# Kernel optimization log

Measured on AMD Instinct MI355X. Metric: run time of the kernel, lower is better.

Reference implementation:

```python
import jax, jax.numpy as jnp
import numpy as np

D_MODEL = 1024
D_FF = 4096
LN_EPS = 1e-5


def _layer_norm(x, gamma, beta):
    mu = jnp.mean(x, axis=-1, keepdims=True)
    var = jnp.mean(jnp.square(x - mu), axis=-1, keepdims=True)
    return (x - mu) * jax.lax.rsqrt(var + LN_EPS) * gamma + beta


def setup_inputs() -> dict:
    key = jax.random.key(0)
    ks = jax.random.split(key, 16)
    B, S, D, F = 2, 2048, D_MODEL, D_FF
    s_d = 1.0 / np.sqrt(D)
    s_f = 1.0 / np.sqrt(F)
    u = lambda k, shape, s: jax.random.uniform(k, shape, jnp.float32, -s, s)
    return {
        "x": jax.random.normal(ks[0], (B, S, D), jnp.float32),
        "wq": u(ks[1], (D, D), s_d), "bq": u(ks[2], (D,), s_d),
        "wk": u(ks[3], (D, D), s_d), "bk": u(ks[4], (D,), s_d),
        "wv": u(ks[5], (D, D), s_d), "bv": u(ks[6], (D,), s_d),
        "wo": u(ks[7], (D, D), s_d), "bo": u(ks[8], (D,), s_d),
        "w1": u(ks[9], (F, D), s_d), "b1": u(ks[10], (F,), s_d),
        "w2": u(ks[11], (D, F), s_f), "b2": u(ks[12], (D,), s_f),
        "g1": jnp.ones((D,), jnp.float32), "be1": jnp.zeros((D,), jnp.float32),
        "g2": jnp.ones((D,), jnp.float32), "be2": jnp.zeros((D,), jnp.float32),
        "num_heads": 16,
    }


def reference(x, wq, bq, wk, bk, wv, bv, wo, bo, w1, b1, w2, b2, g1, be1, g2, be2, num_heads):
    B, S, D = x.shape
    H = num_heads
    dk = D // H
    scale = 1.0 / np.sqrt(dk)

    # --- self-attention (pre-norm) ---
    h = _layer_norm(x, g1, be1)
    q = (h @ wq.T + bq).reshape(B, S, H, dk)
    k = (h @ wk.T + bk).reshape(B, S, H, dk)
    v = (h @ wv.T + bv).reshape(B, S, H, dk)
    scores = jnp.einsum("bqhd,bkhd->bhqk", q, k) * scale  # [B,H,S,S]
    attn = jax.nn.softmax(scores, axis=-1)
    ctx = jnp.einsum("bhqk,bkhd->bqhd", attn, v).reshape(B, S, D)
    x = x + ctx @ wo.T + bo

    # --- feed-forward (pre-norm, exact GELU as in torch default) ---
    h = _layer_norm(x, g2, be2)
    h = jax.nn.gelu(h @ w1.T + b1, approximate=False)
    x = x + h @ w2.T + b2
    return x
```

## Files before the change

kernel.cpp:

```cpp
#include <hip/hip_runtime.h>

typedef __attribute__((ext_vector_type(8))) __bf16 bf16x8;
typedef __attribute__((ext_vector_type(4))) __bf16 bf16x4;
typedef __attribute__((ext_vector_type(4))) float floatx4;
typedef void __attribute__((address_space(3))) lds_void_t;
typedef const void __attribute__((address_space(1))) gbl_void_t;

#define D_MODEL 1024
#define SEQ     2048
#define BATCH   2
#define NH      16
#define DK      64
#define DFF     4096
#define NTOK    (BATCH * SEQ)
#define QKVS    3072

__device__ __forceinline__ float gelu_exact(float x) {
    return 0.5f * x * (1.0f + erff(x * 0.70710678118654752f));
}

__global__ __launch_bounds__(256) void cast_f32_bf16(const float* __restrict__ src,
                                                     __bf16* __restrict__ dst, int n) {
    int i = (blockIdx.x * 256 + threadIdx.x) * 8;
    if (i >= n) return;
    floatx4 a = *(const floatx4*)(src + i);
    floatx4 b = *(const floatx4*)(src + i + 4);
    bf16x8 o;
    for (int j = 0; j < 4; ++j) { o[j] = (__bf16)a[j]; o[4 + j] = (__bf16)b[j]; }
    *(bf16x8*)(dst + i) = o;
}

__global__ __launch_bounds__(64) void ln_kernel(const float* __restrict__ x,
                                                const float* __restrict__ g,
                                                const float* __restrict__ b,
                                                __bf16* __restrict__ out) {
    int row = blockIdx.x, lane = threadIdx.x, base = lane * 16;
    const float* xr = x + (size_t)row * D_MODEL + base;
    float v[16];
    for (int j = 0; j < 4; ++j) {
        floatx4 a = *(const floatx4*)(xr + 4 * j);
        for (int i = 0; i < 4; ++i) v[4 * j + i] = a[i];
    }
    float s = 0.f, sq = 0.f;
    for (int i = 0; i < 16; ++i) { s += v[i]; sq += v[i] * v[i]; }
    for (int o = 1; o < 64; o <<= 1) { s += __shfl_xor(s, o); sq += __shfl_xor(sq, o); }
    float mu = s * (1.0f / D_MODEL);
    float var = sq * (1.0f / D_MODEL) - mu * mu;
    float rstd = rsqrtf(fmaxf(var, 0.f) + 1e-5f);

    const floatx4* gp = (const floatx4*)(g + base);
    const floatx4* bp = (const floatx4*)(b + base);
    bf16x8 o0, o1;
    for (int j = 0; j < 2; ++j) {
        floatx4 gv0 = gp[2 * j], gv1 = gp[2 * j + 1];
        floatx4 bv0 = bp[2 * j], bv1 = bp[2 * j + 1];
        for (int i = 0; i < 4; ++i) {
            float r0 = (v[8 * j + i] - mu) * rstd * gv0[i] + bv0[i];
            float r1 = (v[8 * j + 4 + i] - mu) * rstd * gv1[i] + bv1[i];
            if (j == 0) { o0[i] = (__bf16)r0; o0[4 + i] = (__bf16)r1; }
            else        { o1[i] = (__bf16)r0; o1[4 + i] = (__bf16)r1; }
        }
    }
    bf16x8* op = (bf16x8*)(out + (size_t)row * D_MODEL + base);
    op[0] = o0; op[1] = o1;
}

template <typename OutT, bool GELU, bool TRIBIAS, int KSPLIT>
__global__ __launch_bounds__(256) void gemm_bt(const __bf16* __restrict__ A,
                                               const __bf16* __restrict__ W,
                                               const float* __restrict__ bias0,
                                               const float* __restrict__ bias1,
                                               const float* __restrict__ bias2,
                                               const float* __restrict__ res,
                                               OutT* out, float* part1,
                                               int M, int N, int K) {
    __shared__ __bf16 As[2][128][32];
    __shared__ __bf16 Ws[2][128][32];

    int m0 = blockIdx.y * 128, n0 = blockIdx.x * 128;
    int t = threadIdx.x;
    int lane = t & 63, wave = t >> 6;
    int wm = (wave >> 1) * 64, wn = (wave & 1) * 64;
    int fr = lane & 15, quad = lane >> 4;
    int srow = t >> 2, scol = (t & 3) * 8;

    int Ks = K / KSPLIT;
    int kbeg = (KSPLIT > 1) ? blockIdx.z * Ks : 0;

    floatx4 acc[4][4] = {};

    const __bf16* Ab = A + (size_t)(m0 + srow) * K + kbeg + scol;
    const __bf16* Wb = W + (size_t)(n0 + srow) * K + kbeg + scol;

    auto stage = [&](int buf, int k0) {
        __builtin_amdgcn_global_load_lds((gbl_void_t*)(Ab + k0),
                                         (lds_void_t*)&As[buf][wave * 16][0], 16, 0, 0);
        __builtin_amdgcn_global_load_lds((gbl_void_t*)(Ab + (size_t)64 * K + k0),
                                         (lds_void_t*)&As[buf][64 + wave * 16][0], 16, 0, 0);
        __builtin_amdgcn_global_load_lds((gbl_void_t*)(Wb + k0),
                                         (lds_void_t*)&Ws[buf][wave * 16][0], 16, 0, 0);
        __builtin_amdgcn_global_load_lds((gbl_void_t*)(Wb + (size_t)64 * K + k0),
                                         (lds_void_t*)&Ws[buf][64 + wave * 16][0], 16, 0, 0);
    };

    stage(0, 0);
    int nsteps = Ks / 32;
    for (int s = 0; s < nsteps; ++s) {
        int cur = s & 1;
        __syncthreads();
        if (s + 1 < nsteps) stage(cur ^ 1, (s + 1) * 32);

        bf16x8 af[4], wf[4];
#pragma unroll
        for (int i = 0; i < 4; ++i) af[i] = *(const bf16x8*)&As[cur][wm + i * 16 + fr][quad * 8];
#pragma unroll
        for (int i = 0; i < 4; ++i) wf[i] = *(const bf16x8*)&Ws[cur][wn + i * 16 + fr][quad * 8];
#pragma unroll
        for (int mi = 0; mi < 4; ++mi)
#pragma unroll
            for (int ni = 0; ni < 4; ++ni)
                acc[mi][ni] = __builtin_amdgcn_mfma_f32_16x16x32_bf16(af[mi], wf[ni], acc[mi][ni], 0, 0, 0);
    }

    if (KSPLIT > 1) {
        float* pb = (blockIdx.z == 0) ? (float*)out : part1;
#pragma unroll
        for (int ni = 0; ni < 4; ++ni) {
            int col = n0 + wn + ni * 16 + fr;
#pragma unroll
            for (int mi = 0; mi < 4; ++mi)
#pragma unroll
                for (int r = 0; r < 4; ++r) {
                    int row = m0 + wm + mi * 16 + quad * 4 + r;
                    pb[(size_t)row * N + col] = acc[mi][ni][r];
                }
        }
    } else {
#pragma unroll
        for (int ni = 0; ni < 4; ++ni) {
            int col = n0 + wn + ni * 16 + fr;
            const float* bp = bias0;
            int bcol = col;
            if (TRIBIAS) { bp = col < 1024 ? bias0 : (col < 2048 ? bias1 : bias2); bcol = col & 1023; }
            float bv = bp[bcol];
#pragma unroll
            for (int mi = 0; mi < 4; ++mi) {
#pragma unroll
                for (int r = 0; r < 4; ++r) {
                    int row = m0 + wm + mi * 16 + quad * 4 + r;
                    float v = acc[mi][ni][r] + bv;
                    if (GELU) v = gelu_exact(v);
                    if (res) v += res[(size_t)row * N + col];
                    out[(size_t)row * N + col] = (OutT)v;
                }
            }
        }
    }
}

__global__ __launch_bounds__(256) void reduce_k2(const float* __restrict__ p0,
                                                 const float* p1,
                                                 const float* __restrict__ res,
                                                 const float* __restrict__ bias,
                                                 float* out) {
    int i = (blockIdx.x * 256 + threadIdx.x) * 4;
    floatx4 a = *(const floatx4*)(p0 + i);
    floatx4 b = *(const floatx4*)(p1 + i);
    floatx4 r = *(const floatx4*)(res + i);
    floatx4 bv = *(const floatx4*)(bias + (i & 1023));
    floatx4 o;
#pragma unroll
    for (int j = 0; j < 4; ++j) o[j] = a[j] + b[j] + r[j] + bv[j];
    *(floatx4*)(out + i) = o;
}

__global__ __launch_bounds__(256) void transpose_v(const __bf16* __restrict__ qkv,
                                                   __bf16* __restrict__ vt) {
    __shared__ __bf16 tile[64][72];
    int b = blockIdx.z, h = blockIdx.y, s0 = blockIdx.x * 64;
    int t = threadIdx.x;
    int dl = (t & 7) * 8, sl = t >> 3;
    for (int p = 0; p < 2; ++p) {
        int s = sl + p * 32;
        bf16x8 val = *(const bf16x8*)(qkv + (size_t)(b * SEQ + s0 + s) * QKVS + 2048 + h * DK + dl);
        *(bf16x8*)&tile[s][dl] = val;
    }
    __syncthreads();
    int sl2 = (t & 7) * 8, d = t >> 3;
    for (int p = 0; p < 2; ++p) {
        int dd = d + p * 32;
        bf16x8 val;
        for (int j = 0; j < 8; ++j) val[j] = tile[sl2 + j][dd];
        *(bf16x8*)(vt + ((size_t)(b * NH + h) * DK + dd) * SEQ + s0 + sl2) = val;
    }
}

__global__ __launch_bounds__(256, 2) void attn_kernel(const __bf16* __restrict__ qkv,
                                                      const __bf16* __restrict__ vt,
                                                      __bf16* __restrict__ ctx) {
    __shared__ __bf16 Klds[128][64];
    __shared__ __bf16 Vlds[64][128];
    __shared__ __bf16 Plds[4][16][136];
    int b = blockIdx.z, h = blockIdx.y;
    int wave = threadIdx.x >> 6, lane = threadIdx.x & 63;
    int q0 = blockIdx.x * 64 + wave * 16;
    int fr = lane & 15, quad = lane >> 4;
    const float scale = 0.125f;

    const __bf16* qp = qkv + (size_t)(b * SEQ + q0 + fr) * QKVS + h * DK + quad * 8;
    bf16x8 qf0 = *(const bf16x8*)qp;
    bf16x8 qf1 = *(const bf16x8*)(qp + 32);

    const __bf16* kg = qkv + (size_t)b * SEQ * QKVS + 1024 + h * DK;
    const __bf16* vg = vt + (size_t)(b * NH + h) * DK * SEQ;

    int krow = wave * 8 + (lane >> 3);
    int kcbp = (lane & 7) * 16;
    int vrow = wave * 4 + (lane >> 4);
    int vcbp = (lane & 15) * 16;
    int swb = (fr & 7) << 4;

    floatx4 o[4] = {};
    float m_i = -1e30f, l_i = 0.f;

#pragma unroll
    for (int p = 0; p < 4; ++p) {
        int kr = krow + p * 32;
        int vr = vrow + p * 16;
        __builtin_amdgcn_global_load_lds(
            (gbl_void_t*)(kg + (size_t)kr * QKVS + ((kcbp ^ ((kr & 7) << 4)) >> 1)),
            (lds_void_t*)&Klds[p * 32 + wave * 8][0], 16, 0, 0);
        __builtin_amdgcn_global_load_lds(
            (gbl_void_t*)(vg + (size_t)vr * SEQ + ((vcbp ^ ((vr & 7) << 4)) >> 1)),
            (lds_void_t*)&Vlds[p * 16 + wave * 4][0], 16, 0, 0);
    }
    __syncthreads();

    for (int k0 = 0; k0 < SEQ; k0 += 128) {
        bf16x8 kA[8], kB[8];
#pragma unroll
        for (int f = 0; f < 8; ++f) {
            const char* rp = (const char*)&Klds[0][0] + (f * 16 + fr) * 128;
            kA[f] = *(const bf16x8*)(rp + ((quad * 16) ^ swb));
            kB[f] = *(const bf16x8*)(rp + ((64 + quad * 16) ^ swb));
        }
        bf16x8 vf[4][4];
#pragma unroll
        for (int c = 0; c < 4; ++c)
#pragma unroll
            for (int ti = 0; ti < 4; ++ti)
                vf[c][ti] = *(const bf16x8*)((const char*)&Vlds[0][0] +
                                             (ti * 16 + fr) * 256 + ((c * 64 + quad * 16) ^ swb));
        __syncthreads();

        if (k0 + 128 < SEQ) {
#pragma unroll
            for (int p = 0; p < 4; ++p) {
                int kr = krow + p * 32;
                int vr = vrow + p * 16;
                __builtin_amdgcn_global_load_lds(
                    (gbl_void_t*)(kg + (size_t)(k0 + 128 + kr) * QKVS + ((kcbp ^ ((kr & 7) << 4)) >> 1)),
                    (lds_void_t*)&Klds[p * 32 + wave * 8][0], 16, 0, 0);
                __builtin_amdgcn_global_load_lds(
                    (gbl_void_t*)(vg + (size_t)vr * SEQ + k0 + 128 + ((vcbp ^ ((vr & 7) << 4)) >> 1)),
                    (lds_void_t*)&Vlds[p * 16 + wave * 4][0], 16, 0, 0);
            }
        }

        floatx4 s[8];
#pragma unroll
        for (int f = 0; f < 8; ++f) {
            floatx4 z = {0.f, 0.f, 0.f, 0.f};
            z = __builtin_amdgcn_mfma_f32_16x16x32_bf16(kA[f], qf0, z, 0, 0, 0);
            s[f] = __builtin_amdgcn_mfma_f32_16x16x32_bf16(kB[f], qf1, z, 0, 0, 0);
        }

        float mx = s[0][0];
#pragma unroll
        for (int f = 0; f < 8; ++f)
#pragma unroll
            for (int r = 0; r < 4; ++r) mx = fmaxf(mx, s[f][r]);
        mx *= scale;
        mx = fmaxf(mx, __shfl_xor(mx, 16));
        mx = fmaxf(mx, __shfl_xor(mx, 32));
        float mn = fmaxf(m_i, mx);
        float alpha = __expf(m_i - mn);
        m_i = mn;
        float rs = 0.f;
#pragma unroll
        for (int f = 0; f < 8; ++f) {
            bf16x4 pk;
#pragma unroll
            for (int r = 0; r < 4; ++r) {
                float p = __expf(s[f][r] * scale - mn);
                rs += p;
                pk[r] = (__bf16)p;
            }
            *(bf16x4*)&Plds[wave][fr][f * 16 + quad * 4] = pk;
        }
        rs += __shfl_xor(rs, 16);
        rs += __shfl_xor(rs, 32);
        l_i = l_i * alpha + rs;
        float aB[4];
#pragma unroll
        for (int r = 0; r < 4; ++r) aB[r] = __shfl(alpha, quad * 4 + r);
#pragma unroll
        for (int ti = 0; ti < 4; ++ti)
#pragma unroll
            for (int r = 0; r < 4; ++r) o[ti][r] *= aB[r];
        __threadfence_block();

        bf16x8 pa[4];
#pragma unroll
        for (int c = 0; c < 4; ++c)
            pa[c] = *(const bf16x8*)&Plds[wave][fr][c * 32 + quad * 8];
#pragma unroll
        for (int c = 0; c < 4; ++c)
#pragma unroll
            for (int ti = 0; ti < 4; ++ti)
                o[ti] = __builtin_amdgcn_mfma_f32_16x16x32_bf16(pa[c], vf[c][ti], o[ti], 0, 0, 0);
        __threadfence_block();

        __syncthreads();
    }
    float lB[4];
#pragma unroll
    for (int r = 0; r < 4; ++r) lB[r] = __shfl(l_i, quad * 4 + r);
#pragma unroll
    for (int ti = 0; ti < 4; ++ti)
#pragma unroll
        for (int r = 0; r < 4; ++r)
            ctx[(size_t)(b * SEQ + q0 + quad * 4 + r) * D_MODEL + h * DK + ti * 16 + fr] =
                (__bf16)(o[ti][r] / lB[r]);
}

extern "C" void kernel_launch(void* const* d_in, const int* in_sizes, int n_in,
                              void* d_out, int out_size, void* d_ws, size_t ws_size,
                              hipStream_t stream) {
    const float* x   = (const float*)d_in[0];
    const float* wq  = (const float*)d_in[1];
    const float* bq  = (const float*)d_in[2];
    const float* wk  = (const float*)d_in[3];
    const float* bk  = (const float*)d_in[4];
    const float* wv  = (const float*)d_in[5];
    const float* bv  = (const float*)d_in[6];
    const float* wo  = (const float*)d_in[7];
    const float* bo  = (const float*)d_in[8];
    const float* w1  = (const float*)d_in[9];
    const float* b1  = (const float*)d_in[10];
    const float* w2  = (const float*)d_in[11];
    const float* b2  = (const float*)d_in[12];
    const float* g1  = (const float*)d_in[13];
    const float* be1 = (const float*)d_in[14];
    const float* g2  = (const float*)d_in[15];
    const float* be2 = (const float*)d_in[16];
    float* out = (float*)d_out;

    char* ws = (char*)d_ws;
    const size_t MB = 1024 * 1024;
    __bf16* wqkvB = (__bf16*)(ws);
    __bf16* woB   = (__bf16*)(ws + 6 * MB);
    __bf16* w1B   = (__bf16*)(ws + 8 * MB);
    __bf16* w2B   = (__bf16*)(ws + 16 * MB);
    __bf16* h1    = (__bf16*)(ws + 24 * MB);
    float*  x1    = (float*)(ws + 24 * MB);
    __bf16* qkv   = (__bf16*)(ws + 40 * MB);
    __bf16* vt    = (__bf16*)(ws + 64 * MB);
    __bf16* ffh   = (__bf16*)(ws + 40 * MB);
    float*  pA0   = (float*)(ws + 40 * MB);
    float*  pA1   = (float*)(ws + 56 * MB);
    float*  pF0   = (float*)(ws);
    __bf16* ctx   = (__bf16*)d_out;
    __bf16* h2    = (__bf16*)d_out;

    const int NDD = D_MODEL * D_MODEL;
    const int NDF = D_MODEL * DFF;
    cast_f32_bf16<<<NDD / 2048, 256, 0, stream>>>(wq, wqkvB, NDD);
    cast_f32_bf16<<<NDD / 2048, 256, 0, stream>>>(wk, wqkvB + NDD, NDD);
    cast_f32_bf16<<<NDD / 2048, 256, 0, stream>>>(wv, wqkvB + 2 * NDD, NDD);
    cast_f32_bf16<<<NDD / 2048, 256, 0, stream>>>(wo, woB, NDD);
    cast_f32_bf16<<<NDF / 2048, 256, 0, stream>>>(w1, w1B, NDF);
    cast_f32_bf16<<<NDF / 2048, 256, 0, stream>>>(w2, w2B, NDF);

    dim3 gQKV(QKVS / 128, NTOK / 128);
    dim3 gDz(D_MODEL / 128, NTOK / 128, 2);
    dim3 gF(DFF / 128, NTOK / 128);
    dim3 gAttn(SEQ / 64, NH, BATCH);
    int gRed = NTOK * D_MODEL / (256 * 4);

    ln_kernel<<<NTOK, 64, 0, stream>>>(x, g1, be1, h1);
    gemm_bt<__bf16, false, true, 1><<<gQKV, 256, 0, stream>>>(h1, wqkvB, bq, bk, bv, nullptr, qkv, nullptr, NTOK, QKVS, D_MODEL);
    transpose_v<<<gAttn, 256, 0, stream>>>(qkv, vt);
    attn_kernel<<<gAttn, 256, 0, stream>>>(qkv, vt, ctx);
    gemm_bt<float, false, false, 2><<<gDz, 256, 0, stream>>>(ctx, woB, nullptr, nullptr, nullptr, nullptr, pA0, pA1, NTOK, D_MODEL, D_MODEL);
    reduce_k2<<<gRed, 256, 0, stream>>>(pA0, pA1, x, bo, x1);
    ln_kernel<<<NTOK, 64, 0, stream>>>(x1, g2, be2, h2);
    gemm_bt<__bf16, true, false, 1><<<gF, 256, 0, stream>>>(h2, w1B, b1, b1, b1, nullptr, ffh, nullptr, NTOK, DFF, D_MODEL);
    gemm_bt<float, false, false, 2><<<gDz, 256, 0, stream>>>(ffh, w2B, nullptr, nullptr, nullptr, nullptr, pF0, (float*)d_out, NTOK, D_MODEL, DFF);
    reduce_k2<<<gRed, 256, 0, stream>>>(pF0, (float*)d_out, x1, b2, out);
}
```

Measured before the change: 432.5 us.

## Store K/V tiles in MFMA fragment order in LDS and use exp2 softmax

```diff
diff --git a/kernel.cpp b/kernel.cpp
--- a/kernel.cpp
+++ b/kernel.cpp
@@ -14,6 +14,12 @@
 #define DFF     4096
 #define NTOK    (BATCH * SEQ)
 #define QKVS    3072
+
+#if __has_builtin(__builtin_amdgcn_exp2f)
+#define EXP2(x) __builtin_amdgcn_exp2f(x)
+#else
+#define EXP2(x) exp2f(x)
+#endif
 
 __device__ __forceinline__ float gelu_exact(float x) {
     return 0.5f * x * (1.0f + erff(x * 0.70710678118654752f));
@@ -198,14 +204,14 @@
 __global__ __launch_bounds__(256, 2) void attn_kernel(const __bf16* __restrict__ qkv,
                                                       const __bf16* __restrict__ vt,
                                                       __bf16* __restrict__ ctx) {
-    __shared__ __bf16 Klds[128][64];
-    __shared__ __bf16 Vlds[64][128];
+    __shared__ __bf16 Klds[8192];
+    __shared__ __bf16 Vlds[8192];
     __shared__ __bf16 Plds[4][16][136];
     int b = blockIdx.z, h = blockIdx.y;
     int wave = threadIdx.x >> 6, lane = threadIdx.x & 63;
     int q0 = blockIdx.x * 64 + wave * 16;
     int fr = lane & 15, quad = lane >> 4;
-    const float scale = 0.125f;
+    const float sc2 = 0.18033688011112042f;
 
     const __bf16* qp = qkv + (size_t)(b * SEQ + q0 + fr) * QKVS + h * DK + quad * 8;
     bf16x8 qf0 = *(const bf16x8*)qp;
@@ -214,58 +220,45 @@
     const __bf16* kg = qkv + (size_t)b * SEQ * QKVS + 1024 + h * DK;
     const __bf16* vg = vt + (size_t)(b * NH + h) * DK * SEQ;
 
-    int krow = wave * 8 + (lane >> 3);
-    int kcbp = (lane & 7) * 16;
-    int vrow = wave * 4 + (lane >> 4);
-    int vcbp = (lane & 15) * 16;
-    int swb = (fr & 7) << 4;
-
     floatx4 o[4] = {};
     float m_i = -1e30f, l_i = 0.f;
 
-#pragma unroll
-    for (int p = 0; p < 4; ++p) {
-        int kr = krow + p * 32;
-        int vr = vrow + p * 16;
-        __builtin_amdgcn_global_load_lds(
-            (gbl_void_t*)(kg + (size_t)kr * QKVS + ((kcbp ^ ((kr & 7) << 4)) >> 1)),
-            (lds_void_t*)&Klds[p * 32 + wave * 8][0], 16, 0, 0);
-        __builtin_amdgcn_global_load_lds(
-            (gbl_void_t*)(vg + (size_t)vr * SEQ + ((vcbp ^ ((vr & 7) << 4)) >> 1)),
-            (lds_void_t*)&Vlds[p * 16 + wave * 4][0], 16, 0, 0);
-    }
+    auto stage_tile = [&](int k0) {
+#pragma unroll
+        for (int p = 0; p < 4; ++p) {
+            int bid = wave * 4 + p;
+            int f = bid >> 1, half = bid & 1;
+            __builtin_amdgcn_global_load_lds(
+                (gbl_void_t*)(kg + (size_t)(k0 + f * 16 + fr) * QKVS + quad * 8 + half * 32),
+                (lds_void_t*)&Klds[bid * 512], 16, 0, 0);
+            int c = bid >> 2, ti = bid & 3;
+            __builtin_amdgcn_global_load_lds(
+                (gbl_void_t*)(vg + (size_t)(ti * 16 + fr) * SEQ + k0 + c * 32 + quad * 8),
+                (lds_void_t*)&Vlds[bid * 512], 16, 0, 0);
+        }
+    };
+
+    stage_tile(0);
     __syncthreads();
 
     for (int k0 = 0; k0 < SEQ; k0 += 128) {
+        const __bf16* Kb = Klds + lane * 8;
+        const __bf16* Vb = Vlds + lane * 8;
         bf16x8 kA[8], kB[8];
 #pragma unroll
         for (int f = 0; f < 8; ++f) {
-            const char* rp = (const char*)&Klds[0][0] + (f * 16 + fr) * 128;
-            kA[f] = *(const bf16x8*)(rp + ((quad * 16) ^ swb));
-            kB[f] = *(const bf16x8*)(rp + ((64 + quad * 16) ^ swb));
+            kA[f] = *(const bf16x8*)(Kb + (f * 2 + 0) * 512);
+            kB[f] = *(const bf16x8*)(Kb + (f * 2 + 1) * 512);
         }
         bf16x8 vf[4][4];
 #pragma unroll
         for (int c = 0; c < 4; ++c)
 #pragma unroll
             for (int ti = 0; ti < 4; ++ti)
-                vf[c][ti] = *(const bf16x8*)((const char*)&Vlds[0][0] +
-                                             (ti * 16 + fr) * 256 + ((c * 64 + quad * 16) ^ swb));
+                vf[c][ti] = *(const bf16x8*)(Vb + (c * 4 + ti) * 512);
         __syncthreads();
 
-        if (k0 + 128 < SEQ) {
-#pragma unroll
-            for (int p = 0; p < 4; ++p) {
-                int kr = krow + p * 32;
-                int vr = vrow + p * 16;
-                __builtin_amdgcn_global_load_lds(
-                    (gbl_void_t*)(kg + (size_t)(k0 + 128 + kr) * QKVS + ((kcbp ^ ((kr & 7) << 4)) >> 1)),
-                    (lds_void_t*)&Klds[p * 32 + wave * 8][0], 16, 0, 0);
-                __builtin_amdgcn_global_load_lds(
-                    (gbl_void_t*)(vg + (size_t)vr * SEQ + k0 + 128 + ((vcbp ^ ((vr & 7) << 4)) >> 1)),
-                    (lds_void_t*)&Vlds[p * 16 + wave * 4][0], 16, 0, 0);
-            }
-        }
+        if (k0 + 128 < SEQ) stage_tile(k0 + 128);
 
         floatx4 s[8];
 #pragma unroll
@@ -275,29 +268,31 @@
             s[f] = __builtin_amdgcn_mfma_f32_16x16x32_bf16(kB[f], qf1, z, 0, 0, 0);
         }
 
-        float mx = s[0][0];
+        float fm[8];
 #pragma unroll
         for (int f = 0; f < 8; ++f)
-#pragma unroll
-            for (int r = 0; r < 4; ++r) mx = fmaxf(mx, s[f][r]);
-        mx *= scale;
-        mx = fmaxf(mx, __shfl_xor(mx, 16));
-        mx = fmaxf(mx, __shfl_xor(mx, 32));
-        float mn = fmaxf(m_i, mx);
-        float alpha = __expf(m_i - mn);
+            fm[f] = fmaxf(fmaxf(s[f][0], s[f][1]), fmaxf(s[f][2], s[f][3]));
+        float mx = fmaxf(fmaxf(fmaxf(fm[0], fm[1]), fmaxf(fm[2], fm[3])),
+                         fmaxf(fmaxf(fm[4], fm[5]), fmaxf(fm[6], fm[7])));
+        float mx2 = mx * sc2;
+        mx2 = fmaxf(mx2, __shfl_xor(mx2, 16));
+        mx2 = fmaxf(mx2, __shfl_xor(mx2, 32));
+        float mn = fmaxf(m_i, mx2);
+        float alpha = EXP2(m_i - mn);
         m_i = mn;
-        float rs = 0.f;
+        float r0 = 0.f, r1 = 0.f, r2 = 0.f, r3 = 0.f;
 #pragma unroll
         for (int f = 0; f < 8; ++f) {
             bf16x4 pk;
-#pragma unroll
-            for (int r = 0; r < 4; ++r) {
-                float p = __expf(s[f][r] * scale - mn);
-                rs += p;
-                pk[r] = (__bf16)p;
-            }
+            float p0 = EXP2(fmaf(s[f][0], sc2, -mn));
+            float p1 = EXP2(fmaf(s[f][1], sc2, -mn));
+            float p2 = EXP2(fmaf(s[f][2], sc2, -mn));
+            float p3 = EXP2(fmaf(s[f][3], sc2, -mn));
+            r0 += p0; r1 += p1; r2 += p2; r3 += p3;
+            pk[0] = (__bf16)p0; pk[1] = (__bf16)p1; pk[2] = (__bf16)p2; pk[3] = (__bf16)p3;
             *(bf16x4*)&Plds[wave][fr][f * 16 + quad * 4] = pk;
         }
+        float rs = (r0 + r1) + (r2 + r3);
         rs += __shfl_xor(rs, 16);
         rs += __shfl_xor(rs, 32);
         l_i = l_i * alpha + rs;
```

Measured after the change: 432.3 us. No clear change (-0.0%).
